# Performance work log

Measured on AMD Instinct MI355X. Metric: run time of the kernel, lower is better.

Reference implementation:

```python
import jax, jax.numpy as jnp
import numpy as np

EPS = 1e-12  # torch F.normalize default eps


def _l2norm(x):
    return x / jnp.maximum(jnp.linalg.norm(x, axis=-1, keepdims=True), EPS)


def setup_inputs() -> dict:
    key = jax.random.key(0)
    k1, k2, k3, k4 = jax.random.split(key, 4)
    B, N, F = 2048, 128, 256
    drug = jax.random.normal(k1, (B, N, F), dtype=jnp.float32)
    cell = jax.random.normal(k2, (B, F), dtype=jnp.float32)
    # xavier_uniform bound for square [F,F]: sqrt(6/(F+F))
    bound = float(np.sqrt(6.0 / (F + F)))
    k = jax.random.uniform(k3, (F, F), minval=-bound, maxval=bound, dtype=jnp.float32)
    q = jax.random.uniform(k4, (F, F), minval=-bound, maxval=bound, dtype=jnp.float32)
    return {"drug": drug, "cell": cell, "k": k, "q": q}


def reference(drug, cell, k, q):
    d = _l2norm(drug)                 # [B, N, F]
    c = _l2norm(cell[:, None, :])     # [B, 1, F]
    drug_ = d @ k                     # [B, N, F]
    cell_ = c @ q                     # [B, 1, F]
    scores = jnp.einsum('bof,bnf->bon', cell_, drug_)  # [B, 1, N]
    attn = jax.nn.softmax(scores, axis=2)
    sim = jnp.einsum('bof,bnf->bon', c, d)             # [B, 1, N]
    return (attn * sim)[:, 0, :]      # [B, N]
```

## Files before the change

### kernel.cpp

```cpp
#include <hip/hip_runtime.h>
#include <math.h>

#define F 256
#define NROW 128
#define EPS 1e-12f

typedef float vf4 __attribute__((ext_vector_type(4)));

__global__ __launch_bounds__(256) void qkT_kernel(const float* __restrict__ q,
                                                  const float* __restrict__ k,
                                                  float* __restrict__ M) {
    __shared__ float qs[F];
    int f = blockIdx.x;
    qs[threadIdx.x] = q[(size_t)f * F + threadIdx.x];
    __syncthreads();
    int g = threadIdx.x;
    const float4* kr = (const float4*)(k + (size_t)g * F);
    const float4* qr = (const float4*)qs;
    float acc = 0.f;
#pragma unroll 8
    for (int j = 0; j < F / 4; j++) {
        float4 kv = kr[j];
        float4 qv = qr[j];
        acc += kv.x * qv.x + kv.y * qv.y + kv.z * qv.z + kv.w * qv.w;
    }
    M[(size_t)f * F + g] = acc;
}

__global__ __launch_bounds__(256) void w_gemm(const float* __restrict__ cell,
                                              const float* __restrict__ M,
                                              float* __restrict__ W) {
    __shared__ float As[32][64];
    __shared__ float Bs[64][64];
    int rb = blockIdx.x * 32;
    int cb = blockIdx.y * 64;
    int tid = threadIdx.x;
    int wave = tid >> 6;
    int lane = tid & 63;
    float acc[8] = {0.f, 0.f, 0.f, 0.f, 0.f, 0.f, 0.f, 0.f};
    for (int k0 = 0; k0 < F; k0 += 64) {
        __syncthreads();
#pragma unroll
        for (int e = 0; e < 2; e++) {
            int s = tid + e * 256;
            int r = s >> 4;
            int c = (s & 15) << 2;
            *(float4*)&As[r][c] = *(const float4*)&cell[(size_t)(rb + r) * F + k0 + c];
        }
#pragma unroll
        for (int e = 0; e < 4; e++) {
            int s = tid + e * 256;
            int r = s >> 4;
            int c = (s & 15) << 2;
            *(float4*)&Bs[r][c] = *(const float4*)&M[(size_t)(k0 + r) * F + cb + c];
        }
        __syncthreads();
#pragma unroll 4
        for (int kk = 0; kk < 64; kk++) {
            float bv = Bs[kk][lane];
#pragma unroll
            for (int r = 0; r < 8; r++) {
                acc[r] += As[wave * 8 + r][kk] * bv;
            }
        }
    }
#pragma unroll
    for (int r = 0; r < 8; r++) {
        W[(size_t)(rb + wave * 8 + r) * F + cb + lane] = acc[r];
    }
}

__global__ __launch_bounds__(256) void fused_main(const float* __restrict__ drug,
                                                  const float* __restrict__ cell,
                                                  const float* __restrict__ Wraw,
                                                  float* __restrict__ out) {
    int b = blockIdx.x;
    int tid = threadIdx.x;
    int wave = tid >> 6;
    int lane = tid & 63;
    int grp = lane >> 4;
    int l16 = lane & 15;

    __shared__ float sc[NROW];
    __shared__ float sm[NROW];
    __shared__ float red[4];

    const float* wrow = Wraw + (size_t)b * F;
    const float* crow = cell + (size_t)b * F;
    vf4 w4[4], c4[4];
    float cs = 0.f;
#pragma unroll
    for (int j = 0; j < 4; j++) {
        w4[j] = *(const vf4*)&wrow[j * 64 + l16 * 4];
        c4[j] = *(const vf4*)&crow[j * 64 + l16 * 4];
        cs += c4[j].x * c4[j].x + c4[j].y * c4[j].y + c4[j].z * c4[j].z + c4[j].w * c4[j].w;
    }
#pragma unroll
    for (int m = 1; m < 16; m <<= 1) cs += __shfl_xor(cs, m, 64);
    float invc = 1.0f / fmaxf(sqrtf(cs), EPS);

    const float* dbase = drug + (size_t)b * NROW * F;
#pragma unroll 2
    for (int it = 0; it < 8; it++) {
        int n = wave * 32 + it * 4 + grp;
        const float* drow = dbase + (size_t)n * F;
        float an = 0.f, aw = 0.f, ac = 0.f;
#pragma unroll
        for (int j = 0; j < 4; j++) {
            vf4 v = __builtin_nontemporal_load((const vf4*)&drow[j * 64 + l16 * 4]);
            an += v.x * v.x + v.y * v.y + v.z * v.z + v.w * v.w;
            aw += v.x * w4[j].x + v.y * w4[j].y + v.z * w4[j].z + v.w * w4[j].w;
            ac += v.x * c4[j].x + v.y * c4[j].y + v.z * c4[j].z + v.w * c4[j].w;
        }
#pragma unroll
        for (int m = 1; m < 16; m <<= 1) {
            an += __shfl_xor(an, m, 64);
            aw += __shfl_xor(aw, m, 64);
            ac += __shfl_xor(ac, m, 64);
        }
        if (l16 == 0) {
            float inv = invc / fmaxf(sqrtf(an), EPS);
            sc[n] = aw * inv;
            sm[n] = ac * inv;
        }
    }
    __syncthreads();

    float s = sc[tid & 127];
    float v = s;
#pragma unroll
    for (int m = 1; m < 64; m <<= 1) v = fmaxf(v, __shfl_xor(v, m, 64));
    if (lane == 0) red[wave] = v;
    __syncthreads();
    float gmax = fmaxf(fmaxf(red[0], red[1]), fmaxf(red[2], red[3]));
    float e = expf(s - gmax);
    float t = (tid < NROW) ? e : 0.f;
#pragma unroll
    for (int m = 1; m < 64; m <<= 1) t += __shfl_xor(t, m, 64);
    __syncthreads();
    if (lane == 0) red[wave] = t;
    __syncthreads();
    float tot = red[0] + red[1] + red[2] + red[3];
    if (tid < NROW) {
        out[(size_t)b * NROW + tid] = (e / tot) * sm[tid & 127];
    }
}

extern "C" void kernel_launch(void* const* d_in, const int* in_sizes, int n_in,
                              void* d_out, int out_size, void* d_ws, size_t ws_size,
                              hipStream_t stream) {
    const float* drug = (const float*)d_in[0];
    const float* cell = (const float*)d_in[1];
    const float* k = (const float*)d_in[2];
    const float* q = (const float*)d_in[3];
    float* out = (float*)d_out;

    int B = in_sizes[1] / F;

    float* M = (float*)d_ws;
    float* W = M + (size_t)F * F;

    qkT_kernel<<<dim3(F), dim3(256), 0, stream>>>(q, k, M);
    w_gemm<<<dim3(B / 32, F / 64), dim3(256), 0, stream>>>(cell, M, W);
    fused_main<<<dim3(B), dim3(256), 0, stream>>>(drug, cell, W, out);
}
```

Before: 363.6 us.

## Fuse cell-by-M GEMV into main kernel and drop separate W GEMM launch

Removes the standalone w_gemm kernel and computes each batch row's W = c·M inside fused_main. Each of the four waves handles a 64-row slice of M, and the partial results are reduced through shared memory. This drops one kernel launch and the W round trip through global memory. In exchange, every block now reads the full 256KB M matrix, which should mostly hit in L2, and adds two barriers and extra work before the drug streaming starts.

```diff
diff --git a/kernel.cpp b/kernel.cpp
--- a/kernel.cpp
+++ b/kernel.cpp
@@ -27,52 +27,9 @@
     M[(size_t)f * F + g] = acc;
 }
 
-__global__ __launch_bounds__(256) void w_gemm(const float* __restrict__ cell,
-                                              const float* __restrict__ M,
-                                              float* __restrict__ W) {
-    __shared__ float As[32][64];
-    __shared__ float Bs[64][64];
-    int rb = blockIdx.x * 32;
-    int cb = blockIdx.y * 64;
-    int tid = threadIdx.x;
-    int wave = tid >> 6;
-    int lane = tid & 63;
-    float acc[8] = {0.f, 0.f, 0.f, 0.f, 0.f, 0.f, 0.f, 0.f};
-    for (int k0 = 0; k0 < F; k0 += 64) {
-        __syncthreads();
-#pragma unroll
-        for (int e = 0; e < 2; e++) {
-            int s = tid + e * 256;
-            int r = s >> 4;
-            int c = (s & 15) << 2;
-            *(float4*)&As[r][c] = *(const float4*)&cell[(size_t)(rb + r) * F + k0 + c];
-        }
-#pragma unroll
-        for (int e = 0; e < 4; e++) {
-            int s = tid + e * 256;
-            int r = s >> 4;
-            int c = (s & 15) << 2;
-            *(float4*)&Bs[r][c] = *(const float4*)&M[(size_t)(k0 + r) * F + cb + c];
-        }
-        __syncthreads();
-#pragma unroll 4
-        for (int kk = 0; kk < 64; kk++) {
-            float bv = Bs[kk][lane];
-#pragma unroll
-            for (int r = 0; r < 8; r++) {
-                acc[r] += As[wave * 8 + r][kk] * bv;
-            }
-        }
-    }
-#pragma unroll
-    for (int r = 0; r < 8; r++) {
-        W[(size_t)(rb + wave * 8 + r) * F + cb + lane] = acc[r];
-    }
-}
-
 __global__ __launch_bounds__(256) void fused_main(const float* __restrict__ drug,
                                                   const float* __restrict__ cell,
-                                                  const float* __restrict__ Wraw,
+                                                  const float* __restrict__ M,
                                                   float* __restrict__ out) {
     int b = blockIdx.x;
     int tid = threadIdx.x;
@@ -84,20 +41,46 @@
     __shared__ float sc[NROW];
     __shared__ float sm[NROW];
     __shared__ float red[4];
+    __shared__ float wp[4][F];
+    __shared__ float wsh[F];
 
-    const float* wrow = Wraw + (size_t)b * F;
     const float* crow = cell + (size_t)b * F;
-    vf4 w4[4], c4[4];
+
+    {
+        int c = lane;
+        int fp = wave;
+        vf4 acc = {0.f, 0.f, 0.f, 0.f};
+        const float* Mp = M + (size_t)(fp * 64) * F + 4 * c;
+        const float* cp = crow + fp * 64;
+#pragma unroll 8
+        for (int f = 0; f < 64; f++) {
+            vf4 m4 = *(const vf4*)(Mp + (size_t)f * F);
+            float cf = cp[f];
+            acc.x += cf * m4.x;
+            acc.y += cf * m4.y;
+            acc.z += cf * m4.z;
+            acc.w += cf * m4.w;
+        }
+        *(vf4*)&wp[fp][4 * c] = acc;
+    }
+    __syncthreads();
+    wsh[tid] = wp[0][tid] + wp[1][tid] + wp[2][tid] + wp[3][tid];
+
+    vf4 c4[4];
     float cs = 0.f;
 #pragma unroll
     for (int j = 0; j < 4; j++) {
-        w4[j] = *(const vf4*)&wrow[j * 64 + l16 * 4];
         c4[j] = *(const vf4*)&crow[j * 64 + l16 * 4];
         cs += c4[j].x * c4[j].x + c4[j].y * c4[j].y + c4[j].z * c4[j].z + c4[j].w * c4[j].w;
     }
 #pragma unroll
     for (int m = 1; m < 16; m <<= 1) cs += __shfl_xor(cs, m, 64);
     float invc = 1.0f / fmaxf(sqrtf(cs), EPS);
+    __syncthreads();
+
+    vf4 w4[4];
+#pragma unroll
+    for (int j = 0; j < 4; j++) w4[j] = *(const vf4*)&wsh[j * 64 + l16 * 4];
 
     const float* dbase = drug + (size_t)b * NROW * F;
 #pragma unroll 2
@@ -158,9 +141,7 @@
     int B = in_sizes[1] / F;
 
     float* M = (float*)d_ws;
-    float* W = M + (size_t)F * F;
 
     qkT_kernel<<<dim3(F), dim3(256), 0, stream>>>(q, k, M);
-    w_gemm<<<dim3(B / 32, F / 64), dim3(256), 0, stream>>>(cell, M, W);
-    fused_main<<<dim3(B), dim3(256), 0, stream>>>(drug, cell, W, out);
+    fused_main<<<dim3(B), dim3(256), 0, stream>>>(drug, cell, M, out);
 }
```

After: 363.0 us. No clear change (-0.2%).
